# Kernel optimization log

Hardware: AMD Instinct MI355X
Metric: run time of the kernel (lower is better)

## Reference

```python
import jax, jax.numpy as jnp
import numpy as np

T = 8192        # timesteps
IN = 512        # input_size
H = 1024        # hidden_layer_size
OUT = 256       # output_size
STEP = 0.25     # ODE solver step_size
NSUB = 4        # euler substeps per unit time interval (t spacing = 1)


def setup_inputs() -> dict:
    key = jax.random.key(0)
    ks = jax.random.split(key, 16)
    def lin(k, out_d, in_d):
        kw, kb = jax.random.split(k)
        W = jax.random.normal(kw, (out_d, in_d), jnp.float32) / np.sqrt(in_d).astype(np.float32)
        b = jax.random.normal(kb, (out_d, 1), jnp.float32) * 0.01
        return W, b
    W_in, b_in = lin(ks[0], H, IN)      # linear_in
    W_h, b_h = lin(ks[1], H, H)         # linear_hidden
    W_h2, b_h2 = lin(ks[2], H, H)       # linear_hidden2
    W_f1, b_f1 = lin(ks[3], H, H)       # ode_func.linear
    W_f2, b_f2 = lin(ks[4], H, H)       # ode_func.linear2
    W_dec, b_dec = lin(ks[5], OUT, H)   # decoder
    x = jax.random.normal(ks[6], (T, IN, 1), jnp.float32)
    t = jnp.arange(T, dtype=jnp.float32)
    return dict(t=t, x=x, W_in=W_in, b_in=b_in, W_h=W_h, b_h=b_h,
                W_h2=W_h2, b_h2=b_h2, W_f1=W_f1, b_f1=b_f1,
                W_f2=W_f2, b_f2=b_f2, W_dec=W_dec, b_dec=b_dec)


def reference(t, x, W_in, b_in, W_h, b_h, W_h2, b_h2, W_f1, b_f1, W_f2, b_f2, W_dec, b_dec):
    # ODE_Func: f(h) = W_f2 @ tanh(W_f1 @ h + b_f1) + b_f2   (autonomous; t unused)
    def ode_f(h):
        return W_f2 @ jnp.tanh(W_f1 @ h + b_f1) + b_f2

    dts = (t[1:] - t[:-1]) / NSUB  # (T-1,) euler substep sizes (fixed-grid euler)

    def step(h, inp):
        x_i, dt = inp
        # odeint(ode_func, h, t[i-1:i+1], method='euler', step_size=STEP)
        for _ in range(NSUB):
            h = h + dt * ode_f(h)
        # RNN cell update
        pre = W_in @ x_i + b_in + W_h @ h + b_h          # (H,1)
        h_new = jnp.tanh(W_h2 @ jnp.tanh(pre) + b_h2)    # (H,1)
        return h_new, None

    h0 = jnp.zeros((W_h.shape[0], 1), x.dtype)
    # original loop skips i == 0 entirely (h stays zeros there)
    h_T, _ = jax.lax.scan(step, h0, (x[1:], dts))
    return W_dec @ h_T + b_dec  # (OUT, 1)
```

## Files before the change

kernel.cpp:

```cpp
#include <hip/hip_runtime.h>
#include <math.h>


#define TSTEPS 8192
#define INP    512
#define HDIM   1024
#define NWG    64
#define BLK    256

typedef unsigned long long u64;
typedef unsigned int u32;

__device__ __forceinline__ u64 aload(u64* p) {
    return __hip_atomic_load(p, __ATOMIC_RELAXED, __HIP_MEMORY_SCOPE_AGENT);
}
__device__ __forceinline__ void astore(u64* p, u64 v) {
    __hip_atomic_store(p, v, __ATOMIC_RELAXED, __HIP_MEMORY_SCOPE_AGENT);
}
__device__ __forceinline__ u64 pack(u32 tag, float f) {
    return ((u64)tag << 32) | (u64)__float_as_uint(f);
}

__global__ __launch_bounds__(256)
void mm1024(const float* __restrict__ A, const float* __restrict__ B,
            float* __restrict__ C) {
    __shared__ float As[64][17];
    __shared__ float Bs[16][65];
    const int tid = threadIdx.x;
    const int tx = tid & 15, ty = tid >> 4;
    const int r0 = blockIdx.y * 64, c0 = blockIdx.x * 64;
    float acc[4][4] = {};
    for (int k0 = 0; k0 < HDIM; k0 += 16) {
        const int ar = tid >> 2, ac = (tid & 3) * 4;
        const float4 av = *reinterpret_cast<const float4*>(
            A + (size_t)(r0 + ar) * HDIM + k0 + ac);
        As[ar][ac] = av.x; As[ar][ac + 1] = av.y;
        As[ar][ac + 2] = av.z; As[ar][ac + 3] = av.w;
        const int br = tid >> 4, bc = (tid & 15) * 4;
        const float4 bv = *reinterpret_cast<const float4*>(
            B + (size_t)(k0 + br) * HDIM + c0 + bc);
        Bs[br][bc] = bv.x; Bs[br][bc + 1] = bv.y;
        Bs[br][bc + 2] = bv.z; Bs[br][bc + 3] = bv.w;
        __syncthreads();
        #pragma unroll
        for (int kk = 0; kk < 16; ++kk) {
            float a[4], b[4];
            #pragma unroll
            for (int i2 = 0; i2 < 4; ++i2) a[i2] = As[ty * 4 + i2][kk];
            #pragma unroll
            for (int j2 = 0; j2 < 4; ++j2) b[j2] = Bs[kk][tx * 4 + j2];
            #pragma unroll
            for (int i2 = 0; i2 < 4; ++i2)
                #pragma unroll
                for (int j2 = 0; j2 < 4; ++j2)
                    acc[i2][j2] = fmaf(a[i2], b[j2], acc[i2][j2]);
        }
        __syncthreads();
    }
    #pragma unroll
    for (int i2 = 0; i2 < 4; ++i2)
        #pragma unroll
        for (int j2 = 0; j2 < 4; ++j2)
            C[(size_t)(r0 + ty * 4 + i2) * HDIM + c0 + tx * 4 + j2] = acc[i2][j2];
}

__global__ __launch_bounds__(BLK, 1)
void ode_rnn_persistent(
    const float* __restrict__ t,    const float* __restrict__ x,
    const float* __restrict__ W_in, const float* __restrict__ b_in,
    const float* __restrict__ W_h,  const float* __restrict__ b_h,
    const float* __restrict__ W_h2, const float* __restrict__ b_h2,
    const float* __restrict__ W_f1, const float* __restrict__ b_f1,
    const float* __restrict__ b_f2,
    const float* __restrict__ W_dec, const float* __restrict__ b_dec,
    const float* __restrict__ Mw,   const float* __restrict__ Pw,
    float* __restrict__ out,
    u64* QA, u64* QB, u64* QC, u64* QD)
{
    extern __shared__ float smem[];
    float* wh2l = smem;
    float* wf1l = smem + 16 * 1024;
    float* sb0  = smem + 32 * 1024;
    float* sb1  = sb0 + 1024;
    float* sb2  = sb1 + 1024;
    float* us   = sb2 + 1024;

    const int tid  = threadIdx.x;
    const int wg   = blockIdx.x;
    const int seg  = tid & 15;
    const int rloc = tid >> 4;
    const int row  = wg * 16 + rloc;

    {
        const float* s2 = W_h2 + (size_t)wg * 16 * HDIM;
        const float* s1 = W_f1 + (size_t)wg * 16 * HDIM;
        for (int k = 0; k < 16; ++k) {
            const int idx = k * 1024 + tid * 4;
            *reinterpret_cast<float4*>(wh2l + idx) =
                *reinterpret_cast<const float4*>(s2 + idx);
            *reinterpret_cast<float4*>(wf1l + idx) =
                *reinterpret_cast<const float4*>(s1 + idx);
        }
    }

    float4 m16[16], p16[16], whr[16], wir[8], xr[8];
    {
        const float4* pM = reinterpret_cast<const float4*>(Mw  + (size_t)row * HDIM);
        const float4* pP = reinterpret_cast<const float4*>(Pw  + (size_t)row * HDIM);
        const float4* pH = reinterpret_cast<const float4*>(W_h + (size_t)row * HDIM);
        #pragma unroll
        for (int j = 0; j < 16; ++j) {
            m16[j] = pM[j * 16 + seg];
            p16[j] = pP[j * 16 + seg];
            whr[j] = pH[j * 16 + seg];
        }
        const float4* pI = reinterpret_cast<const float4*>(W_in + (size_t)row * INP);
        #pragma unroll
        for (int j = 0; j < 8; ++j) wir[j] = pI[j * 16 + seg];
        const float4* xp = reinterpret_cast<const float4*>(x + (size_t)1 * INP);
        #pragma unroll
        for (int j = 0; j < 8; ++j) xr[j] = xp[j * 16 + seg];
    }

    const float bf1_r = b_f1[row];
    const float bih_r = b_in[row] + b_h[row];
    const float bh2_r = b_h2[row];

    auto red16 = [&](float a) {
        #pragma unroll
        for (int off = 8; off; off >>= 1) a += __shfl_xor(a, off, 16);
        return a;
    };
    auto dotReg = [&](const float4* w, const float* v) {
        float a = 0.f;
        #pragma unroll
        for (int j = 0; j < 16; ++j) {
            const float4 vv = *reinterpret_cast<const float4*>(v + j * 64 + seg * 4);
            a = fmaf(w[j].x, vv.x, a); a = fmaf(w[j].y, vv.y, a);
            a = fmaf(w[j].z, vv.z, a); a = fmaf(w[j].w, vv.w, a);
        }
        return red16(a);
    };
    auto dotW = [&](const float* Wl, const float* v) {
        const float* wr = Wl + rloc * 1024;
        float a = 0.f;
        #pragma unroll
        for (int j = 0; j < 16; ++j) {
            const float4 w  = *reinterpret_cast<const float4*>(wr + j * 64 + seg * 4);
            const float4 vv = *reinterpret_cast<const float4*>(v  + j * 64 + seg * 4);
            a = fmaf(w.x, vv.x, a); a = fmaf(w.y, vv.y, a);
            a = fmaf(w.z, vv.z, a); a = fmaf(w.w, vv.w, a);
        }
        return red16(a);
    };
    auto pub = [&](u64* q, u32 e, float pre) {
        if (seg == 0) astore(&q[row], pack(e, tanhf(pre)));
    };

    int pb = 0;
    auto stage = [&](u64* q, u32 tag, int mode) -> float* {
        float* dst = (pb == 0) ? sb0 : (pb == 1) ? sb1 : sb2;
        pb = (pb == 2) ? 0 : pb + 1;
        const int i0 = tid, i1 = tid + 256, i2 = tid + 512, i3 = tid + 768;
        u64 A0 = aload(q + i0), A1 = aload(q + i1), A2 = aload(q + i2), A3 = aload(q + i3);
        u64 B0 = aload(q + i0), B1 = aload(q + i1), B2 = aload(q + i2), B3 = aload(q + i3);
        u64 r0, r1, r2, r3;
        for (;;) {
            bool ok = ((u32)(A0 >> 32) == tag) & ((u32)(A1 >> 32) == tag) &
                      ((u32)(A2 >> 32) == tag) & ((u32)(A3 >> 32) == tag);
            if (__all(ok)) { r0 = A0; r1 = A1; r2 = A2; r3 = A3; break; }
            A0 = aload(q + i0); A1 = aload(q + i1); A2 = aload(q + i2); A3 = aload(q + i3);
            ok = ((u32)(B0 >> 32) == tag) & ((u32)(B1 >> 32) == tag) &
                 ((u32)(B2 >> 32) == tag) & ((u32)(B3 >> 32) == tag);
            if (__all(ok)) { r0 = B0; r1 = B1; r2 = B2; r3 = B3; break; }
            B0 = aload(q + i0); B1 = aload(q + i1); B2 = aload(q + i2); B3 = aload(q + i3);
        }
        const float v0 = __uint_as_float((u32)r0), v1 = __uint_as_float((u32)r1);
        const float v2 = __uint_as_float((u32)r2), v3 = __uint_as_float((u32)r3);
        dst[i0] = v0; dst[i1] = v1; dst[i2] = v2; dst[i3] = v3;
        if (mode == 1)      { us[i0]  = v0; us[i1]  = v1; us[i2]  = v2; us[i3]  = v3; }
        else if (mode == 2) { us[i0] += v0; us[i1] += v1; us[i2] += v2; us[i3] += v3; }
        __syncthreads();
        return dst;
    };

    __syncthreads();
    #pragma unroll
    for (int k = 0; k < 4; ++k) sb0[tid + k * 256] = b_f2[tid + k * 256];
    __syncthreads();
    const float c1_own = dotW(wf1l, sb0);
    const float c2_own = dotReg(whr, sb0);
    __syncthreads();

    float z_own = bf1_r;
    float yd_own = 0.f;
    u32 eA = 0, eB = 0, eC = 0, eD = 0;
    float* hprev = sb0;

    #pragma unroll 1
    for (int i = 1; i < TSTEPS; ++i) {
        const float dt = (t[i] - t[i - 1]) * 0.25f;

        ++eA;
        pub(QA, eA, z_own);
        float* b1 = stage(QA, eA, 1);
        z_own = fmaf(dt, dotReg(m16, b1) + c1_own, z_own);

        ++eB;
        pub(QB, eB, z_own);
        if (i > 1) yd_own = dotReg(whr, hprev);
        float* b2 = stage(QB, eB, 2);
        z_own = fmaf(dt, dotReg(m16, b2) + c1_own, z_own);

        ++eA;
        pub(QA, eA, z_own);
        float* b3 = stage(QA, eA, 2);
        z_own = fmaf(dt, dotReg(m16, b3) + c1_own, z_own);

        ++eB;
        pub(QB, eB, z_own);
        float winx;
        {
            float a = 0.f;
            #pragma unroll
            for (int j = 0; j < 8; ++j) {
                a = fmaf(wir[j].x, xr[j].x, a); a = fmaf(wir[j].y, xr[j].y, a);
                a = fmaf(wir[j].z, xr[j].z, a); a = fmaf(wir[j].w, xr[j].w, a);
            }
            winx = red16(a);
        }
        stage(QB, eB, 2);
        const float pd = dotReg(p16, us);
        const float apre = fmaf(dt, pd + 4.f * c2_own, yd_own) + winx + bih_r;

        ++eC;
        pub(QC, eC, apre);
        float* b5 = stage(QC, eC, 0);
        const float hpre = dotW(wh2l, b5) + bh2_r;

        ++eD;
        pub(QD, eD, hpre);
        {
            const int inext = (i + 1 < TSTEPS) ? i + 1 : i;
            const float4* xp = reinterpret_cast<const float4*>(x + (size_t)inext * INP);
            #pragma unroll
            for (int j = 0; j < 8; ++j) xr[j] = xp[j * 16 + seg];
        }
        float* b6 = stage(QD, eD, 0);
        hprev = b6;
        z_own = dotW(wf1l, b6) + bf1_r;
    }

    {
        const int rl = tid >> 6, s2 = tid & 63;
        const int orow = wg * 4 + rl;
        const float4* wd = reinterpret_cast<const float4*>(W_dec + (size_t)orow * HDIM);
        float acc = 0.f;
        #pragma unroll
        for (int j = 0; j < 4; ++j) {
            const float4 w = wd[j * 64 + s2];
            const float4 v = *reinterpret_cast<const float4*>(hprev + j * 256 + s2 * 4);
            acc = fmaf(w.x, v.x, acc); acc = fmaf(w.y, v.y, acc);
            acc = fmaf(w.z, v.z, acc); acc = fmaf(w.w, v.w, acc);
        }
        #pragma unroll
        for (int off = 32; off; off >>= 1) acc += __shfl_down(acc, off, 64);
        if (s2 == 0) out[orow] = acc + b_dec[orow];
    }
}

extern "C" void kernel_launch(void* const* d_in, const int* in_sizes, int n_in,
                              void* d_out, int out_size, void* d_ws, size_t ws_size,
                              hipStream_t stream) {
    const float* t     = (const float*)d_in[0];
    const float* x     = (const float*)d_in[1];
    const float* W_in  = (const float*)d_in[2];
    const float* b_in  = (const float*)d_in[3];
    const float* W_h   = (const float*)d_in[4];
    const float* b_h   = (const float*)d_in[5];
    const float* W_h2  = (const float*)d_in[6];
    const float* b_h2  = (const float*)d_in[7];
    const float* W_f1  = (const float*)d_in[8];
    const float* b_f1  = (const float*)d_in[9];
    const float* W_f2  = (const float*)d_in[10];
    const float* b_f2  = (const float*)d_in[11];
    const float* W_dec = (const float*)d_in[12];
    const float* b_dec = (const float*)d_in[13];
    float* out = (float*)d_out;

    unsigned char* ws = (unsigned char*)d_ws;
    float* Mw = (float*)(ws);
    float* Pw = (float*)(ws + (size_t)4 * 1024 * 1024);
    u64*   QA = (u64*)(ws + (size_t)8 * 1024 * 1024);
    u64*   QB = QA + HDIM;
    u64*   QC = QB + HDIM;
    u64*   QD = QC + HDIM;

    mm1024<<<dim3(16, 16), 256, 0, stream>>>(W_f1, W_f2, Mw);
    mm1024<<<dim3(16, 16), 256, 0, stream>>>(W_h,  W_f2, Pw);

    hipMemsetAsync(ws + (size_t)8 * 1024 * 1024, 0, 4 * HDIM * sizeof(u64), stream);

    const size_t smem_bytes = (size_t)(32 * 1024 + 4 * 1024) * sizeof(float);
    ode_rnn_persistent<<<dim3(NWG), dim3(BLK), smem_bytes, stream>>>(
        t, x, W_in, b_in, W_h, b_h, W_h2, b_h2, W_f1, b_f1, b_f2,
        W_dec, b_dec, Mw, Pw, out, QA, QB, QC, QD);
}
```

Measured before the change: 109.1 ms.

## Pin persistent RNN to a single XCD with L2-local flag polling

Launches 256 blocks and keeps the 32 that land on the first XCD to fill up, so all inter-block flag exchange stays within one XCD's L2. Inside the loop, flag loads and stores use sc0 inline asm (L2-coherent only) instead of device-scope atomics, after a self-test that checks cross-block visibility. Each worker now owns 32 rows. W_f1 and W_h rows are streamed from global memory with prefetch hints instead of being held in LDS or registers, which frees space for the larger per-block tile. The aim is lower per-step synchronisation latency. The cost is fewer compute units, more global weight traffic, and a fragile XCD-selection handshake with a fallback path.

```diff
diff --git a/kernel.cpp b/kernel.cpp
--- a/kernel.cpp
+++ b/kernel.cpp
@@ -5,8 +5,12 @@
 #define TSTEPS 8192
 #define INP    512
 #define HDIM   1024
-#define NWG    64
+#define GRID   256
 #define BLK    256
+#define NWRK   32
+#define RPW    32
+#define SEGN   8
+#define F4PT   32
 
 typedef unsigned long long u64;
 typedef unsigned int u32;
@@ -19,6 +23,24 @@
 }
 __device__ __forceinline__ u64 pack(u32 tag, float f) {
     return ((u64)tag << 32) | (u64)__float_as_uint(f);
+}
+
+__device__ __forceinline__ void sePoll4(const u64* p0, const u64* p1,
+                                        const u64* p2, const u64* p3,
+                                        u64& v0, u64& v1, u64& v2, u64& v3) {
+    asm volatile(
+        "global_load_dwordx2 %0, %4, off sc0\n\t"
+        "global_load_dwordx2 %1, %5, off sc0\n\t"
+        "global_load_dwordx2 %2, %6, off sc0\n\t"
+        "global_load_dwordx2 %3, %7, off sc0\n\t"
+        "s_waitcnt vmcnt(0)"
+        : "=&v"(v0), "=&v"(v1), "=&v"(v2), "=&v"(v3)
+        : "v"(p0), "v"(p1), "v"(p2), "v"(p3)
+        : "memory");
+}
+__device__ __forceinline__ void seStore(u64* p, u64 v) {
+    asm volatile("global_store_dwordx2 %0, %1, off sc0"
+                 :: "v"(p), "v"(v) : "memory");
 }
 
 __global__ __launch_bounds__(256)
@@ -65,7 +87,7 @@
 }
 
 __global__ __launch_bounds__(BLK, 1)
-void ode_rnn_persistent(
+void ode_rnn_xcd(
     const float* __restrict__ t,    const float* __restrict__ x,
     const float* __restrict__ W_in, const float* __restrict__ b_in,
     const float* __restrict__ W_h,  const float* __restrict__ b_h,
@@ -75,127 +97,236 @@
     const float* __restrict__ W_dec, const float* __restrict__ b_dec,
     const float* __restrict__ Mw,   const float* __restrict__ Pw,
     float* __restrict__ out,
-    u64* QA, u64* QB, u64* QC, u64* QD)
+    u64* QA, u64* QB, u64* QC, u64* QD, u64* QT,
+    int* cnt, int* fail_cnt, int* barc, int* chosen)
 {
     extern __shared__ float smem[];
     float* wh2l = smem;
-    float* wf1l = smem + 16 * 1024;
-    float* sb0  = smem + 32 * 1024;
-    float* sb1  = sb0 + 1024;
-    float* sb2  = sb1 + 1024;
-    float* us   = sb2 + 1024;
-
-    const int tid  = threadIdx.x;
-    const int wg   = blockIdx.x;
-    const int seg  = tid & 15;
-    const int rloc = tid >> 4;
-    const int row  = wg * 16 + rloc;
+    float* sb0  = smem + RPW * HDIM;
+    float* sb1  = sb0 + HDIM;
+    float* sb2  = sb1 + HDIM;
+    float* us   = sb2 + HDIM;
+    float* xb   = us + HDIM;
+
+    __shared__ int s_role, s_cand, s_ok[4];
+    const int tid = threadIdx.x;
+
+    if (tid == 0) {
+        u32 xcc;
+        asm volatile("s_getreg_b32 %0, hwreg(HW_REG_XCC_ID)" : "=s"(xcc));
+        xcc &= 7;
+        const int slot = atomicAdd(&cnt[xcc], 1);
+        if (slot == NWRK - 1) atomicCAS(chosen, -1, (int)xcc);
+        int c = -1;
+        for (int it = 0; it < (1 << 20); ++it) {
+            c = __hip_atomic_load(chosen, __ATOMIC_RELAXED,
+                                  __HIP_MEMORY_SCOPE_AGENT);
+            if (c != -1) break;
+        }
+        if (c == -1) {
+            atomicCAS(chosen, -1, 8);
+            do {
+                c = __hip_atomic_load(chosen, __ATOMIC_RELAXED,
+                                      __HIP_MEMORY_SCOPE_AGENT);
+            } while (c == -1);
+        }
+        if (c == 8) { s_role = (blockIdx.x < NWRK) ? (int)blockIdx.x : -1; s_cand = 0; }
+        else        { s_role = (c == (int)xcc && slot < NWRK) ? slot : -1;  s_cand = 1; }
+    }
+    __syncthreads();
+    const int  w    = s_role;
+    const bool cand = (s_cand != 0);
+    if (w < 0) return;
+
+    const int seg  = tid & (SEGN - 1);
+    const int rloc = tid >> 3;
+    const int row  = w * RPW + rloc;
+
+    bool lm = false;
+    if (cand) {
+        int okl = 1;
+        for (u32 tr = 1; tr <= 2; ++tr) {
+            if (okl) {
+                if (seg == 0) seStore(&QT[row], pack(tr, 1.0f));
+                u64 *q0 = QT + tid, *q1 = QT + tid + 256,
+                    *q2 = QT + tid + 512, *q3 = QT + tid + 768;
+                int sweeps = 0;
+                for (;;) {
+                    u64 v0, v1, v2, v3;
+                    sePoll4(q0, q1, q2, q3, v0, v1, v2, v3);
+                    const bool ok =
+                        ((u32)(v0 >> 32) >= tr) & ((u32)(v1 >> 32) >= tr) &
+                        ((u32)(v2 >> 32) >= tr) & ((u32)(v3 >> 32) >= tr);
+                    if (__all(ok)) break;
+                    if (++sweeps > (1 << 16)) { okl = 0; break; }
+                }
+            }
+        }
+        if ((tid & 63) == 0) s_ok[tid >> 6] = okl;
+        __syncthreads();
+        if (tid == 0) {
+            const int o = s_ok[0] & s_ok[1] & s_ok[2] & s_ok[3];
+            if (!o) atomicAdd(fail_cnt, 1);
+            __threadfence();
+            atomicAdd(barc, 1);
+            int b;
+            do {
+                b = __hip_atomic_load(barc, __ATOMIC_RELAXED,
+                                      __HIP_MEMORY_SCOPE_AGENT);
+            } while (b < NWRK);
+            __threadfence();
+            s_cand = (__hip_atomic_load(fail_cnt, __ATOMIC_RELAXED,
+                                        __HIP_MEMORY_SCOPE_AGENT) == 0) ? 1 : 0;
+        }
+        __syncthreads();
+        lm = (s_cand != 0);
+    }
 
     {
-        const float* s2 = W_h2 + (size_t)wg * 16 * HDIM;
-        const float* s1 = W_f1 + (size_t)wg * 16 * HDIM;
-        for (int k = 0; k < 16; ++k) {
-            const int idx = k * 1024 + tid * 4;
-            *reinterpret_cast<float4*>(wh2l + idx) =
-                *reinterpret_cast<const float4*>(s2 + idx);
-            *reinterpret_cast<float4*>(wf1l + idx) =
-                *reinterpret_cast<const float4*>(s1 + idx);
-        }
-    }
-
-    float4 m16[16], p16[16], whr[16], wir[8], xr[8];
+        const float4* src = reinterpret_cast<const float4*>(
+            W_h2 + (size_t)w * RPW * HDIM);
+        float4* dst = reinterpret_cast<float4*>(wh2l);
+        for (int k = tid; k < RPW * HDIM / 4; k += BLK) dst[k] = src[k];
+    }
+
+    float4 m32[F4PT], p32[F4PT];
     {
-        const float4* pM = reinterpret_cast<const float4*>(Mw  + (size_t)row * HDIM);
-        const float4* pP = reinterpret_cast<const float4*>(Pw  + (size_t)row * HDIM);
-        const float4* pH = reinterpret_cast<const float4*>(W_h + (size_t)row * HDIM);
-        #pragma unroll
-        for (int j = 0; j < 16; ++j) {
-            m16[j] = pM[j * 16 + seg];
-            p16[j] = pP[j * 16 + seg];
-            whr[j] = pH[j * 16 + seg];
-        }
-        const float4* pI = reinterpret_cast<const float4*>(W_in + (size_t)row * INP);
-        #pragma unroll
-        for (int j = 0; j < 8; ++j) wir[j] = pI[j * 16 + seg];
-        const float4* xp = reinterpret_cast<const float4*>(x + (size_t)1 * INP);
-        #pragma unroll
-        for (int j = 0; j < 8; ++j) xr[j] = xp[j * 16 + seg];
+        const float4* pM = reinterpret_cast<const float4*>(Mw + (size_t)row * HDIM);
+        const float4* pP = reinterpret_cast<const float4*>(Pw + (size_t)row * HDIM);
+        #pragma unroll
+        for (int j = 0; j < F4PT; ++j) {
+            m32[j] = pM[j * SEGN + seg];
+            p32[j] = pP[j * SEGN + seg];
+        }
     }
 
     const float bf1_r = b_f1[row];
     const float bih_r = b_in[row] + b_h[row];
     const float bh2_r = b_h2[row];
 
-    auto red16 = [&](float a) {
-        #pragma unroll
-        for (int off = 8; off; off >>= 1) a += __shfl_xor(a, off, 16);
+    auto red8 = [&](float a) {
+        #pragma unroll
+        for (int off = 4; off; off >>= 1) a += __shfl_xor(a, off, SEGN);
         return a;
     };
-    auto dotReg = [&](const float4* w, const float* v) {
+    auto dotReg = [&](const float4 (&wr)[F4PT], const float* v) {
         float a = 0.f;
         #pragma unroll
+        for (int j = 0; j < F4PT; ++j) {
+            const float4 vv = *reinterpret_cast<const float4*>(
+                v + (j * SEGN + seg) * 4);
+            a = fmaf(wr[j].x, vv.x, a); a = fmaf(wr[j].y, vv.y, a);
+            a = fmaf(wr[j].z, vv.z, a); a = fmaf(wr[j].w, vv.w, a);
+        }
+        return red8(a);
+    };
+    auto dotLdsW = [&](const float* v) {
+        const float* wr = wh2l + rloc * HDIM;
+        float a = 0.f;
+        #pragma unroll
+        for (int j = 0; j < F4PT; ++j) {
+            const int e = (j * SEGN + seg) * 4;
+            const float4 wv = *reinterpret_cast<const float4*>(wr + e);
+            const float4 vv = *reinterpret_cast<const float4*>(v + e);
+            a = fmaf(wv.x, vv.x, a); a = fmaf(wv.y, vv.y, a);
+            a = fmaf(wv.z, vv.z, a); a = fmaf(wv.w, vv.w, a);
+        }
+        return red8(a);
+    };
+    auto dotStreamPart = [&](const float* Wb, const float* v, int c0, int c1,
+                             float a) {
+        const float4* wp = reinterpret_cast<const float4*>(Wb + (size_t)row * HDIM);
+        for (int c = c0; c < c1; c += 8) {
+            float4 wreg[8];
+            #pragma unroll
+            for (int j = 0; j < 8; ++j) wreg[j] = wp[(c + j) * SEGN + seg];
+            #pragma unroll
+            for (int j = 0; j < 8; ++j) {
+                const float4 vv = *reinterpret_cast<const float4*>(
+                    v + ((c + j) * SEGN + seg) * 4);
+                a = fmaf(wreg[j].x, vv.x, a); a = fmaf(wreg[j].y, vv.y, a);
+                a = fmaf(wreg[j].z, vv.z, a); a = fmaf(wreg[j].w, vv.w, a);
+            }
+        }
+        return a;
+    };
+    auto prefRow = [&](const float* Wb, int c0) {
+        const float4* wp = reinterpret_cast<const float4*>(Wb + (size_t)row * HDIM);
+        #pragma unroll
         for (int j = 0; j < 16; ++j) {
-            const float4 vv = *reinterpret_cast<const float4*>(v + j * 64 + seg * 4);
-            a = fmaf(w[j].x, vv.x, a); a = fmaf(w[j].y, vv.y, a);
-            a = fmaf(w[j].z, vv.z, a); a = fmaf(w[j].w, vv.w, a);
-        }
-        return red16(a);
-    };
-    auto dotW = [&](const float* Wl, const float* v) {
-        const float* wr = Wl + rloc * 1024;
+            const float4 wv = wp[(c0 + j) * SEGN + seg];
+            asm volatile("" :: "v"(wv.x), "v"(wv.y), "v"(wv.z), "v"(wv.w));
+        }
+    };
+    auto dotWinx = [&]() {
+        const float4* wp = reinterpret_cast<const float4*>(W_in + (size_t)row * INP);
         float a = 0.f;
         #pragma unroll
         for (int j = 0; j < 16; ++j) {
-            const float4 w  = *reinterpret_cast<const float4*>(wr + j * 64 + seg * 4);
-            const float4 vv = *reinterpret_cast<const float4*>(v  + j * 64 + seg * 4);
-            a = fmaf(w.x, vv.x, a); a = fmaf(w.y, vv.y, a);
-            a = fmaf(w.z, vv.z, a); a = fmaf(w.w, vv.w, a);
-        }
-        return red16(a);
+            const float4 wv = wp[j * SEGN + seg];
+            const float4 vv = *reinterpret_cast<const float4*>(
+                xb + (j * SEGN + seg) * 4);
+            a = fmaf(wv.x, vv.x, a); a = fmaf(wv.y, vv.y, a);
+            a = fmaf(wv.z, vv.z, a); a = fmaf(wv.w, vv.w, a);
+        }
+        return red8(a);
     };
     auto pub = [&](u64* q, u32 e, float pre) {
-        if (seg == 0) astore(&q[row], pack(e, tanhf(pre)));
+        if (seg == 0) {
+            const u64 pv = pack(e, tanhf(pre));
+            if (lm) seStore(&q[row], pv);
+            else    astore(&q[row], pv);
+        }
     };
 
     int pb = 0;
     auto stage = [&](u64* q, u32 tag, int mode) -> float* {
         float* dst = (pb == 0) ? sb0 : (pb == 1) ? sb1 : sb2;
         pb = (pb == 2) ? 0 : pb + 1;
-        const int i0 = tid, i1 = tid + 256, i2 = tid + 512, i3 = tid + 768;
-        u64 A0 = aload(q + i0), A1 = aload(q + i1), A2 = aload(q + i2), A3 = aload(q + i3);
-        u64 B0 = aload(q + i0), B1 = aload(q + i1), B2 = aload(q + i2), B3 = aload(q + i3);
-        u64 r0, r1, r2, r3;
-        for (;;) {
-            bool ok = ((u32)(A0 >> 32) == tag) & ((u32)(A1 >> 32) == tag) &
-                      ((u32)(A2 >> 32) == tag) & ((u32)(A3 >> 32) == tag);
-            if (__all(ok)) { r0 = A0; r1 = A1; r2 = A2; r3 = A3; break; }
-            A0 = aload(q + i0); A1 = aload(q + i1); A2 = aload(q + i2); A3 = aload(q + i3);
-            ok = ((u32)(B0 >> 32) == tag) & ((u32)(B1 >> 32) == tag) &
-                 ((u32)(B2 >> 32) == tag) & ((u32)(B3 >> 32) == tag);
-            if (__all(ok)) { r0 = B0; r1 = B1; r2 = B2; r3 = B3; break; }
-            B0 = aload(q + i0); B1 = aload(q + i1); B2 = aload(q + i2); B3 = aload(q + i3);
-        }
-        const float v0 = __uint_as_float((u32)r0), v1 = __uint_as_float((u32)r1);
-        const float v2 = __uint_as_float((u32)r2), v3 = __uint_as_float((u32)r3);
-        dst[i0] = v0; dst[i1] = v1; dst[i2] = v2; dst[i3] = v3;
-        if (mode == 1)      { us[i0]  = v0; us[i1]  = v1; us[i2]  = v2; us[i3]  = v3; }
-        else if (mode == 2) { us[i0] += v0; us[i1] += v1; us[i2] += v2; us[i3] += v3; }
+        u64 *q0 = q + tid, *q1 = q + tid + 256, *q2 = q + tid + 512,
+            *q3 = q + tid + 768;
+        u64 v0, v1, v2, v3;
+        if (lm) {
+            for (;;) {
+                sePoll4(q0, q1, q2, q3, v0, v1, v2, v3);
+                const bool ok =
+                    ((u32)(v0 >> 32) == tag) & ((u32)(v1 >> 32) == tag) &
+                    ((u32)(v2 >> 32) == tag) & ((u32)(v3 >> 32) == tag);
+                if (__all(ok)) break;
+            }
+        } else {
+            for (;;) {
+                v0 = aload(q0); v1 = aload(q1); v2 = aload(q2); v3 = aload(q3);
+                const bool ok =
+                    ((u32)(v0 >> 32) == tag) & ((u32)(v1 >> 32) == tag) &
+                    ((u32)(v2 >> 32) == tag) & ((u32)(v3 >> 32) == tag);
+                if (ok) break;
+            }
+        }
+        const float f0 = __uint_as_float((u32)v0), f1 = __uint_as_float((u32)v1);
+        const float f2 = __uint_as_float((u32)v2), f3 = __uint_as_float((u32)v3);
+        dst[tid] = f0; dst[tid + 256] = f1; dst[tid + 512] = f2; dst[tid + 768] = f3;
+        if (mode == 1) {
+            us[tid] = f0; us[tid + 256] = f1; us[tid + 512] = f2; us[tid + 768] = f3;
+        } else if (mode == 2) {
+            us[tid] += f0; us[tid + 256] += f1; us[tid + 512] += f2; us[tid + 768] += f3;
+        }
         __syncthreads();
         return dst;
     };
 
     __syncthreads();
-    #pragma unroll
-    for (int k = 0; k < 4; ++k) sb0[tid + k * 256] = b_f2[tid + k * 256];
+    for (int k = tid; k < HDIM; k += BLK) sb0[k] = b_f2[k];
+    reinterpret_cast<float2*>(xb)[tid] =
+        reinterpret_cast<const float2*>(x + (size_t)1 * INP)[tid];
     __syncthreads();
-    const float c1_own = dotW(wf1l, sb0);
-    const float c2_own = dotReg(whr, sb0);
+    const float c1_own = red8(dotStreamPart(W_f1, sb0, 0, 32, 0.f));
+    const float c2_own = red8(dotStreamPart(W_h,  sb0, 0, 32, 0.f));
     __syncthreads();
 
     float z_own = bf1_r;
-    float yd_own = 0.f;
     u32 eA = 0, eB = 0, eC = 0, eD = 0;
-    float* hprev = sb0;
+    float* hbuf = sb0;
 
     #pragma unroll 1
     for (int i = 1; i < TSTEPS; ++i) {
@@ -203,68 +334,63 @@
 
         ++eA;
         pub(QA, eA, z_own);
+        float ydacc = 0.f;
+        if (i > 1) ydacc = dotStreamPart(W_h, hbuf, 0, 16, 0.f);
         float* b1 = stage(QA, eA, 1);
-        z_own = fmaf(dt, dotReg(m16, b1) + c1_own, z_own);
+        z_own = fmaf(dt, dotReg(m32, b1) + c1_own, z_own);
 
         ++eB;
         pub(QB, eB, z_own);
-        if (i > 1) yd_own = dotReg(whr, hprev);
+        if (i > 1) ydacc = dotStreamPart(W_h, hbuf, 16, 32, ydacc);
+        const float yd = red8(ydacc);
         float* b2 = stage(QB, eB, 2);
-        z_own = fmaf(dt, dotReg(m16, b2) + c1_own, z_own);
+        z_own = fmaf(dt, dotReg(m32, b2) + c1_own, z_own);
 
         ++eA;
         pub(QA, eA, z_own);
+        prefRow(W_f1, 0);
         float* b3 = stage(QA, eA, 2);
-        z_own = fmaf(dt, dotReg(m16, b3) + c1_own, z_own);
+        z_own = fmaf(dt, dotReg(m32, b3) + c1_own, z_own);
 
         ++eB;
         pub(QB, eB, z_own);
-        float winx;
-        {
-            float a = 0.f;
-            #pragma unroll
-            for (int j = 0; j < 8; ++j) {
-                a = fmaf(wir[j].x, xr[j].x, a); a = fmaf(wir[j].y, xr[j].y, a);
-                a = fmaf(wir[j].z, xr[j].z, a); a = fmaf(wir[j].w, xr[j].w, a);
-            }
-            winx = red16(a);
-        }
+        const float winx = dotWinx();
         stage(QB, eB, 2);
-        const float pd = dotReg(p16, us);
-        const float apre = fmaf(dt, pd + 4.f * c2_own, yd_own) + winx + bih_r;
+        const float pd = dotReg(p32, us);
+        const float apre = fmaf(dt, pd + 4.f * c2_own, yd) + winx + bih_r;
 
         ++eC;
         pub(QC, eC, apre);
+        prefRow(W_f1, 16);
         float* b5 = stage(QC, eC, 0);
-        const float hpre = dotW(wh2l, b5) + bh2_r;
+        const float hpre = dotLdsW(b5) + bh2_r;
 
         ++eD;
         pub(QD, eD, hpre);
-        {
-            const int inext = (i + 1 < TSTEPS) ? i + 1 : i;
-            const float4* xp = reinterpret_cast<const float4*>(x + (size_t)inext * INP);
-            #pragma unroll
-            for (int j = 0; j < 8; ++j) xr[j] = xp[j * 16 + seg];
-        }
+        if (i + 1 < TSTEPS)
+            reinterpret_cast<float2*>(xb)[tid] =
+                reinterpret_cast<const float2*>(x + (size_t)(i + 1) * INP)[tid];
         float* b6 = stage(QD, eD, 0);
-        hprev = b6;
-        z_own = dotW(wf1l, b6) + bf1_r;
+        hbuf = b6;
+        z_own = red8(dotStreamPart(W_f1, b6, 0, 32, 0.f)) + bf1_r;
     }
 
     {
-        const int rl = tid >> 6, s2 = tid & 63;
-        const int orow = wg * 4 + rl;
-        const float4* wd = reinterpret_cast<const float4*>(W_dec + (size_t)orow * HDIM);
+        const int rl = tid >> 5, s2 = tid & 31;
+        const int orow = w * 8 + rl;
+        const float4* wd = reinterpret_cast<const float4*>(
+            W_dec + (size_t)orow * HDIM);
         float acc = 0.f;
         #pragma unroll
-        for (int j = 0; j < 4; ++j) {
-            const float4 w = wd[j * 64 + s2];
-            const float4 v = *reinterpret_cast<const float4*>(hprev + j * 256 + s2 * 4);
-            acc = fmaf(w.x, v.x, acc); acc = fmaf(w.y, v.y, acc);
-            acc = fmaf(w.z, v.z, acc); acc = fmaf(w.w, v.w, acc);
-        }
-        #pragma unroll
-        for (int off = 32; off; off >>= 1) acc += __shfl_down(acc, off, 64);
+        for (int j = 0; j < 8; ++j) {
+            const float4 wv = wd[j * 32 + s2];
+            const float4 vv = *reinterpret_cast<const float4*>(
+                hbuf + (j * 32 + s2) * 4);
+            acc = fmaf(wv.x, vv.x, acc); acc = fmaf(wv.y, vv.y, acc);
+            acc = fmaf(wv.z, vv.z, acc); acc = fmaf(wv.w, vv.w, acc);
+        }
+        #pragma unroll
+        for (int off = 16; off; off >>= 1) acc += __shfl_xor(acc, off, 32);
         if (s2 == 0) out[orow] = acc + b_dec[orow];
     }
 }
@@ -295,14 +421,23 @@
     u64*   QB = QA + HDIM;
     u64*   QC = QB + HDIM;
     u64*   QD = QC + HDIM;
+    u64*   QT = QD + HDIM;
+    int*   cnt      = (int*)(QT + HDIM);
+    int*   fail_cnt = cnt + 8;
+    int*   barc     = cnt + 9;
+    int*   chosen   = cnt + 10;
 
     mm1024<<<dim3(16, 16), 256, 0, stream>>>(W_f1, W_f2, Mw);
     mm1024<<<dim3(16, 16), 256, 0, stream>>>(W_h,  W_f2, Pw);
 
-    hipMemsetAsync(ws + (size_t)8 * 1024 * 1024, 0, 4 * HDIM * sizeof(u64), stream);
-
-    const size_t smem_bytes = (size_t)(32 * 1024 + 4 * 1024) * sizeof(float);
-    ode_rnn_persistent<<<dim3(NWG), dim3(BLK), smem_bytes, stream>>>(
+    hipMemsetAsync(ws + (size_t)8 * 1024 * 1024, 0,
+                   (size_t)5 * HDIM * sizeof(u64) + 10 * sizeof(int), stream);
+    hipMemsetAsync(chosen, 0xFF, sizeof(int), stream);
+
+    const size_t smem_bytes =
+        (size_t)(RPW * HDIM + 3 * HDIM + HDIM + INP) * sizeof(float);
+    ode_rnn_xcd<<<dim3(GRID), dim3(BLK), smem_bytes, stream>>>(
         t, x, W_in, b_in, W_h, b_h, W_h2, b_h2, W_f1, b_f1, b_f2,
-        W_dec, b_dec, Mw, Pw, out, QA, QB, QC, QD);
-}
+        W_dec, b_dec, Mw, Pw, out, QA, QB, QC, QD, QT,
+        cnt, fail_cnt, barc, chosen);
+}
```

After: 431.6 ms. 295% more time.
